# Kernel tuning notes

Measured on AMD Instinct MI355X. Metric: run time of the kernel, lower is better.

## Reference

```python
import jax, jax.numpy as jnp
import numpy as np

TEMP = 0.07
EPS = 1e-6

B = 8192
D1 = 129  # d+1 ambient Lorentz coords


def setup_inputs() -> dict:
    key = jax.random.key(0)
    k1, k2 = jax.random.split(key)
    z1 = jax.random.normal(k1, (B, D1), dtype=jnp.float32)
    z2 = jax.random.normal(k2, (B, D1), dtype=jnp.float32)
    return {"z1": z1, "z2": z2}


def _loss(z1, z2):
    # Minkowski (Lorentz) inner product via a single GEMM:
    # <x,y>_L = -x0*y0 + sum_i xi*yi  ->  x @ (metric * y)^T
    metric = jnp.concatenate([-jnp.ones((1,), z1.dtype), jnp.ones((D1 - 1,), z1.dtype)])
    inner = jnp.einsum('bd,kd->bk', z1, z2 * metric)  # (B, B)
    # Lorentz distance with curvature c=1: acosh(clamp(-<x,y>_L, 1+eps))
    dist = jnp.arccosh(jnp.clip(-inner, 1.0 + EPS, None))
    sims = -dist / TEMP
    # symmetric InfoNCE: labels are the diagonal
    logp_t2i = jax.nn.log_softmax(sims, axis=-1)      # text -> image
    logp_i2t = jax.nn.log_softmax(sims.T, axis=-1)    # image -> text
    diag = jnp.arange(sims.shape[0])
    loss_t2i = -jnp.mean(logp_t2i[diag, diag])
    loss_i2t = -jnp.mean(logp_i2t[diag, diag])
    return (loss_t2i + loss_i2t) / 2.0


def reference(z1, z2):
    return _loss(z1, z2)
```

## Files before the change

kernel.cpp:

```cpp
#include <hip/hip_runtime.h>
#include <math.h>


#define BDIM   8192
#define K_IN   129
#define K_PAD  160
#define BK     32
#define NKT    5
#define CTILES 8

typedef __bf16  bf16x8 __attribute__((ext_vector_type(8)));
typedef float   f32x4  __attribute__((ext_vector_type(4)));
typedef unsigned short u16x4 __attribute__((ext_vector_type(4)));

#define OFF_A    0u
#define OFF_B    (BDIM * K_PAD * 2u)
#define OFF_RS   (2u * BDIM * K_PAD * 2u)
#define OFF_CP   (OFF_RS + BDIM * 4u)
#define OFF_DG   (OFF_CP + 4u * BDIM * 4u)

__device__ __forceinline__ float fast_sqrt(float x) {
#if __has_builtin(__builtin_amdgcn_sqrtf)
    return __builtin_amdgcn_sqrtf(x);
#else
    return sqrtf(x);
#endif
}
__device__ __forceinline__ float fast_log2(float x) {
#if __has_builtin(__builtin_amdgcn_logf)
    return __builtin_amdgcn_logf(x);
#else
    return __log2f(x);
#endif
}
__device__ __forceinline__ float fast_exp2(float x) {
#if __has_builtin(__builtin_amdgcn_exp2f)
    return __builtin_amdgcn_exp2f(x);
#else
    extern "C" __device__ float __ocml_native_exp2_f32(float);
    return __ocml_native_exp2_f32(x);
#endif
}

__device__ __forceinline__ unsigned short f2bf_rne(float f) {
    unsigned int u = __float_as_uint(f);
    u += 0x7FFFu + ((u >> 16) & 1u);
    return (unsigned short)(u >> 16);
}

__global__ __launch_bounds__(256) void convert_kernel(
    const float* __restrict__ z1, const float* __restrict__ z2,
    unsigned short* __restrict__ A, unsigned short* __restrict__ B,
    float* __restrict__ rs_cp)
{
    int v = blockIdx.x * 256 + threadIdx.x;
    if (v < 5 * BDIM) rs_cp[v] = 0.f;
    if (v >= BDIM * (K_PAD / 4)) return;
    int r  = v / (K_PAD / 4);
    int c4 = (v - r * (K_PAD / 4)) * 4;
    u16x4 a, b;
    #pragma unroll
    for (int i = 0; i < 4; ++i) {
        int c = c4 + i;
        float va = 0.f, vb = 0.f;
        if (c < K_IN) {
            va = z1[r * K_IN + c];
            vb = z2[r * K_IN + c];
            if (c == 0) va = -va;
        }
        a[i] = f2bf_rne(va);
        b[i] = f2bf_rne(vb);
    }
    *(u16x4*)(A + r * K_PAD + c4) = a;
    *(u16x4*)(B + r * K_PAD + c4) = b;
}


#define STAGE(bufidx, cb)                                                     \
    {                                                                         \
        const char* _gp = (const char*)(B + (size_t)(cb) * K_PAD)             \
                          + lane * 16;                                        \
        char* _lp = (char*)&Bs[bufidx][0];                                    \
        __builtin_amdgcn_global_load_lds(                                     \
            (const __attribute__((address_space(1))) void*)                   \
                (_gp + wave * 1024),                                          \
            (__attribute__((address_space(3))) void*)(_lp + wave * 1024),     \
            16, 0, 0);                                                        \
        __builtin_amdgcn_global_load_lds(                                     \
            (const __attribute__((address_space(1))) void*)                   \
                (_gp + (wave + 8) * 1024),                                    \
            (__attribute__((address_space(3))) void*)(_lp + (wave + 8) * 1024),\
            16, 0, 0);                                                        \
        if (wave < 4)                                                         \
            __builtin_amdgcn_global_load_lds(                                 \
                (const __attribute__((address_space(1))) void*)               \
                    (_gp + (wave + 16) * 1024),                               \
                (__attribute__((address_space(3))) void*)(_lp + (wave + 16) * 1024),\
                16, 0, 0);                                                    \
    }

#define COMPUTE(bufidx, cb)                                                   \
    {                                                                         \
        const int colBase = (cb);                                             \
        const unsigned short* _Bt = &Bs[bufidx][0];                           \
        f32x4 acc[2][4] = {};                                                 \
        _Pragma("unroll")                                                     \
        for (int kt = 0; kt < NKT; ++kt) {                                    \
            bf16x8 bfr[4];                                                    \
            _Pragma("unroll")                                                 \
            for (int j = 0; j < 4; ++j)                                       \
                bfr[j] = *(const bf16x8*)                                     \
                    &_Bt[(l16 + j * 16) * K_PAD + quad * 8 + kt * BK];        \
            _Pragma("unroll")                                                 \
            for (int i = 0; i < 2; ++i)                                       \
                _Pragma("unroll")                                             \
                for (int j = 0; j < 4; ++j)                                   \
                    acc[i][j] = __builtin_amdgcn_mfma_f32_16x16x32_bf16(      \
                        Ah[i][kt], bfr[j], acc[i][j], 0, 0, 0);               \
        }                                                                     \
        const bool diagTile = (colBase == (rowBase & ~63));                   \
        const int  dj       = (rowBase >> 4) & 2;                             \
        float colp[4] = {0.f, 0.f, 0.f, 0.f};                                 \
        _Pragma("unroll")                                                     \
        for (int i = 0; i < 2; ++i) {                                         \
            _Pragma("unroll")                                                 \
            for (int j = 0; j < 4; ++j) {                                     \
                _Pragma("unroll")                                             \
                for (int reg = 0; reg < 4; ++reg) {                           \
                    float inner = acc[i][j][reg];                             \
                    float x = fmaxf(-inner, 1.000001f);                       \
                    float s = fast_sqrt(__builtin_fmaf(x, x, -1.0f));         \
                    float l2u = fast_log2(x + s);                             \
                    float e = fast_exp2(-14.285714285714286f * l2u);          \
                    rowp[i][reg] += e;                                        \
                    colp[j]      += e;                                        \
                    if (diagTile && (j - i) == dj && (quad * 4 + reg) == l16){\
                        int R = rowBase + i * 16 + quad * 4 + reg;            \
                        diag[R] = -9.902102579427789f * l2u;                  \
                    }                                                         \
                }                                                             \
            }                                                                 \
        }                                                                     \
        _Pragma("unroll")                                                     \
        for (int j = 0; j < 4; ++j) {                                         \
            float v = colp[j];                                                \
            v += __shfl_xor(v, 16);                                           \
            v += __shfl_xor(v, 32);                                           \
            if (quad == 0)                                                    \
                atomicAdd(&colRep[colBase + j * 16 + l16], v);                \
        }                                                                     \
    }

__global__ __launch_bounds__(512, 4) void gemm_epilogue_kernel(
    const unsigned short* __restrict__ A, const unsigned short* __restrict__ B,
    float* __restrict__ row_sum, float* __restrict__ col_part,
    float* __restrict__ diag)
{
    const int t    = threadIdx.x;
    const int lane = t & 63;
    const int wave = t >> 6;
    const int quad = lane >> 4;
    const int l16  = lane & 15;

    const int strip = blockIdx.x & 31;
    const int chunk = blockIdx.x >> 5;
    const int rowBase  = strip * 256 + wave * 32;
    const int colChunk = chunk * 512;

    const unsigned short* Abase = A + (rowBase + l16) * K_PAD + quad * 8;
    float* colRep = col_part + (strip & 3) * BDIM;

    __shared__ __align__(16) unsigned short Bs[2][64 * K_PAD];

    bf16x8 Ah[2][NKT];
    #pragma unroll
    for (int i = 0; i < 2; ++i)
        #pragma unroll
        for (int kt = 0; kt < NKT; ++kt)
            Ah[i][kt] = *(const bf16x8*)(Abase + i * 16 * K_PAD + kt * BK);

    float rowp[2][4] = {};

    STAGE(0, colChunk);
    __syncthreads();

    #pragma unroll 1
    for (int ct = 0; ct < CTILES; ++ct) {
        if (ct + 1 < CTILES)
            STAGE((ct + 1) & 1, colChunk + (ct + 1) * 64);
        COMPUTE(ct & 1, colChunk + ct * 64);
        __syncthreads();
    }

    #pragma unroll
    for (int i = 0; i < 2; ++i) {
        #pragma unroll
        for (int reg = 0; reg < 4; ++reg) {
            float v = rowp[i][reg];
            v += __shfl_xor(v, 1);
            v += __shfl_xor(v, 2);
            v += __shfl_xor(v, 4);
            v += __shfl_xor(v, 8);
            if (l16 == 0)
                atomicAdd(&row_sum[rowBase + i * 16 + quad * 4 + reg], v);
        }
    }
}

__global__ __launch_bounds__(1024) void finalize_kernel(
    const float* __restrict__ rs, const float* __restrict__ cp,
    const float* __restrict__ dg, float* __restrict__ out)
{
    __shared__ float part[16];
    int t = threadIdx.x;
    float a = 0.f;
    const float LN2_HALF = 0.34657359027997264f;
    for (int b = t; b < BDIM; b += 1024) {
        float cs = cp[b] + cp[b + BDIM] + cp[b + 2 * BDIM] + cp[b + 3 * BDIM];
        a += LN2_HALF * (fast_log2(rs[b]) + fast_log2(cs)) - dg[b];
    }
    #pragma unroll
    for (int m = 1; m < 64; m <<= 1) a += __shfl_xor(a, m);
    if ((t & 63) == 0) part[t >> 6] = a;
    __syncthreads();
    if (t < 16) {
        float v = part[t];
        #pragma unroll
        for (int m = 1; m < 16; m <<= 1) v += __shfl_xor(v, m);
        if (t == 0) out[0] = v * (1.0f / (float)BDIM);
    }
}

extern "C" void kernel_launch(void* const* d_in, const int* in_sizes, int n_in,
                              void* d_out, int out_size, void* d_ws, size_t ws_size,
                              hipStream_t stream)
{
    const float* z1 = (const float*)d_in[0];
    const float* z2 = (const float*)d_in[1];
    float* out = (float*)d_out;

    char* ws = (char*)d_ws;
    unsigned short* A  = (unsigned short*)(ws + OFF_A);
    unsigned short* B  = (unsigned short*)(ws + OFF_B);
    float* row_sum     = (float*)(ws + OFF_RS);
    float* col_part    = (float*)(ws + OFF_CP);
    float* diag        = (float*)(ws + OFF_DG);

    convert_kernel<<<(BDIM * (K_PAD / 4) + 255) / 256, 256, 0, stream>>>(
        z1, z2, A, B, row_sum );

    gemm_epilogue_kernel<<<512, 512, 0, stream>>>(
        A, B, row_sum, col_part, diag);

    finalize_kernel<<<1, 1024, 0, stream>>>(row_sum, col_part, diag, out);
}
```

Measured before the change: 108.7 us.

## Fuse convert, GEMM epilogue and finalize into one persistent kernel with grid barriers

Merges the three kernel launches into a single 512-block kernel. The kernel converts inputs to bf16 with a grid-stride loop, waits at a software grid barrier, runs the GEMM/epilogue, waits at a second barrier, and then computes a distributed final reduction with an atomicAdd into the output. The goal is to remove launch gaps and the single-block finalize tail. In exchange it adds a hipMemsetAsync for the barrier counters and relies on all 512 blocks being co-resident, otherwise the barrier spin deadlocks.

After: 199.5 us. 83.5% more time.

```diff
diff --git a/kernel.cpp b/kernel.cpp
--- a/kernel.cpp
+++ b/kernel.cpp
@@ -8,6 +8,8 @@
 #define BK     32
 #define NKT    5
 #define CTILES 8
+#define GRID   512
+#define NTHR   512
 
 typedef __bf16  bf16x8 __attribute__((ext_vector_type(8)));
 typedef float   f32x4  __attribute__((ext_vector_type(4)));
@@ -18,6 +20,7 @@
 #define OFF_RS   (2u * BDIM * K_PAD * 2u)
 #define OFF_CP   (OFF_RS + BDIM * 4u)
 #define OFF_DG   (OFF_CP + 4u * BDIM * 4u)
+#define OFF_SYNC (OFF_DG + BDIM * 4u)
 
 __device__ __forceinline__ float fast_sqrt(float x) {
 #if __has_builtin(__builtin_amdgcn_sqrtf)
@@ -48,37 +51,23 @@
     return (unsigned short)(u >> 16);
 }
 
-__global__ __launch_bounds__(256) void convert_kernel(
-    const float* __restrict__ z1, const float* __restrict__ z2,
-    unsigned short* __restrict__ A, unsigned short* __restrict__ B,
-    float* __restrict__ rs_cp)
-{
-    int v = blockIdx.x * 256 + threadIdx.x;
-    if (v < 5 * BDIM) rs_cp[v] = 0.f;
-    if (v >= BDIM * (K_PAD / 4)) return;
-    int r  = v / (K_PAD / 4);
-    int c4 = (v - r * (K_PAD / 4)) * 4;
-    u16x4 a, b;
-    #pragma unroll
-    for (int i = 0; i < 4; ++i) {
-        int c = c4 + i;
-        float va = 0.f, vb = 0.f;
-        if (c < K_IN) {
-            va = z1[r * K_IN + c];
-            vb = z2[r * K_IN + c];
-            if (c == 0) va = -va;
-        }
-        a[i] = f2bf_rne(va);
-        b[i] = f2bf_rne(vb);
-    }
-    *(u16x4*)(A + r * K_PAD + c4) = a;
-    *(u16x4*)(B + r * K_PAD + c4) = b;
+__device__ __forceinline__ void grid_barrier(unsigned int* cnt) {
+    __syncthreads();
+    if (threadIdx.x == 0) {
+        __threadfence();
+        atomicAdd(cnt, 1u);
+        while (__hip_atomic_load(cnt, __ATOMIC_RELAXED,
+                                 __HIP_MEMORY_SCOPE_AGENT) < GRID)
+            __builtin_amdgcn_s_sleep(2);
+        __threadfence();
+    }
+    __syncthreads();
 }
 
 
 #define STAGE(bufidx, cb)                                                     \
     {                                                                         \
-        const char* _gp = (const char*)(B + (size_t)(cb) * K_PAD)             \
+        const char* _gp = (const char*)(Bp + (size_t)(cb) * K_PAD)            \
                           + lane * 16;                                        \
         char* _lp = (char*)&Bs[bufidx][0];                                    \
         __builtin_amdgcn_global_load_lds(                                     \
@@ -151,83 +140,108 @@
         }                                                                     \
     }
 
-__global__ __launch_bounds__(512, 4) void gemm_epilogue_kernel(
-    const unsigned short* __restrict__ A, const unsigned short* __restrict__ B,
+__global__ __launch_bounds__(NTHR, 4) void fused_kernel(
+    const float* __restrict__ z1, const float* __restrict__ z2,
+    unsigned short* __restrict__ A, unsigned short* __restrict__ Bp,
     float* __restrict__ row_sum, float* __restrict__ col_part,
-    float* __restrict__ diag)
+    float* __restrict__ diag, unsigned int* __restrict__ sync0,
+    unsigned int* __restrict__ sync1, float* __restrict__ out)
 {
-    const int t    = threadIdx.x;
-    const int lane = t & 63;
-    const int wave = t >> 6;
-    const int quad = lane >> 4;
-    const int l16  = lane & 15;
-
-    const int strip = blockIdx.x & 31;
-    const int chunk = blockIdx.x >> 5;
-    const int rowBase  = strip * 256 + wave * 32;
-    const int colChunk = chunk * 512;
-
-    const unsigned short* Abase = A + (rowBase + l16) * K_PAD + quad * 8;
-    float* colRep = col_part + (strip & 3) * BDIM;
-
-    __shared__ __align__(16) unsigned short Bs[2][64 * K_PAD];
-
-    bf16x8 Ah[2][NKT];
-    #pragma unroll
-    for (int i = 0; i < 2; ++i)
+    const int t   = threadIdx.x;
+    const int bid = blockIdx.x;
+
+    {
+        int tidg = bid * NTHR + t;
+        if (tidg < 5 * BDIM) row_sum[tidg] = 0.f;
+        if (tidg == 0) out[0] = 0.f;
+        for (int v = tidg; v < BDIM * (K_PAD / 4); v += GRID * NTHR) {
+            int r  = v / (K_PAD / 4);
+            int c4 = (v - r * (K_PAD / 4)) * 4;
+            u16x4 a, b;
+            #pragma unroll
+            for (int i = 0; i < 4; ++i) {
+                int c = c4 + i;
+                float va = 0.f, vb = 0.f;
+                if (c < K_IN) {
+                    va = z1[r * K_IN + c];
+                    vb = z2[r * K_IN + c];
+                    if (c == 0) va = -va;
+                }
+                a[i] = f2bf_rne(va);
+                b[i] = f2bf_rne(vb);
+            }
+            *(u16x4*)(A + r * K_PAD + c4)  = a;
+            *(u16x4*)(Bp + r * K_PAD + c4) = b;
+        }
+    }
+
+    grid_barrier(sync0);
+
+    {
+        const int lane = t & 63;
+        const int wave = t >> 6;
+        const int quad = lane >> 4;
+        const int l16  = lane & 15;
+
+        const int strip = bid & 31;
+        const int chunk = bid >> 5;
+        const int rowBase  = strip * 256 + wave * 32;
+        const int colChunk = chunk * 512;
+
+        const unsigned short* Abase = A + (rowBase + l16) * K_PAD + quad * 8;
+        float* colRep = col_part + (strip & 3) * BDIM;
+
+        __shared__ __align__(16) unsigned short Bs[2][64 * K_PAD];
+
+        bf16x8 Ah[2][NKT];
         #pragma unroll
-        for (int kt = 0; kt < NKT; ++kt)
-            Ah[i][kt] = *(const bf16x8*)(Abase + i * 16 * K_PAD + kt * BK);
-
-    float rowp[2][4] = {};
-
-    STAGE(0, colChunk);
-    __syncthreads();
-
-    #pragma unroll 1
-    for (int ct = 0; ct < CTILES; ++ct) {
-        if (ct + 1 < CTILES)
-            STAGE((ct + 1) & 1, colChunk + (ct + 1) * 64);
-        COMPUTE(ct & 1, colChunk + ct * 64);
+        for (int i = 0; i < 2; ++i)
+            #pragma unroll
+            for (int kt = 0; kt < NKT; ++kt)
+                Ah[i][kt] = *(const bf16x8*)(Abase + i * 16 * K_PAD + kt * BK);
+
+        float rowp[2][4] = {};
+
+        STAGE(0, colChunk);
         __syncthreads();
-    }
-
-    #pragma unroll
-    for (int i = 0; i < 2; ++i) {
+
+        #pragma unroll 1
+        for (int ct = 0; ct < CTILES; ++ct) {
+            if (ct + 1 < CTILES)
+                STAGE((ct + 1) & 1, colChunk + (ct + 1) * 64);
+            COMPUTE(ct & 1, colChunk + ct * 64);
+            __syncthreads();
+        }
+
         #pragma unroll
-        for (int reg = 0; reg < 4; ++reg) {
-            float v = rowp[i][reg];
-            v += __shfl_xor(v, 1);
-            v += __shfl_xor(v, 2);
-            v += __shfl_xor(v, 4);
-            v += __shfl_xor(v, 8);
-            if (l16 == 0)
-                atomicAdd(&row_sum[rowBase + i * 16 + quad * 4 + reg], v);
+        for (int i = 0; i < 2; ++i) {
+            #pragma unroll
+            for (int reg = 0; reg < 4; ++reg) {
+                float v = rowp[i][reg];
+                v += __shfl_xor(v, 1);
+                v += __shfl_xor(v, 2);
+                v += __shfl_xor(v, 4);
+                v += __shfl_xor(v, 8);
+                if (l16 == 0)
+                    atomicAdd(&row_sum[rowBase + i * 16 + quad * 4 + reg], v);
+            }
         }
     }
-}
-
-__global__ __launch_bounds__(1024) void finalize_kernel(
-    const float* __restrict__ rs, const float* __restrict__ cp,
-    const float* __restrict__ dg, float* __restrict__ out)
-{
-    __shared__ float part[16];
-    int t = threadIdx.x;
-    float a = 0.f;
-    const float LN2_HALF = 0.34657359027997264f;
-    for (int b = t; b < BDIM; b += 1024) {
-        float cs = cp[b] + cp[b + BDIM] + cp[b + 2 * BDIM] + cp[b + 3 * BDIM];
-        a += LN2_HALF * (fast_log2(rs[b]) + fast_log2(cs)) - dg[b];
-    }
-    #pragma unroll
-    for (int m = 1; m < 64; m <<= 1) a += __shfl_xor(a, m);
-    if ((t & 63) == 0) part[t >> 6] = a;
-    __syncthreads();
+
+    grid_barrier(sync1);
+
     if (t < 16) {
-        float v = part[t];
-        #pragma unroll
-        for (int m = 1; m < 16; m <<= 1) v += __shfl_xor(v, m);
-        if (t == 0) out[0] = v * (1.0f / (float)BDIM);
+        const float LN2_HALF = 0.34657359027997264f;
+        int b = bid * 16 + t;
+        float cs = col_part[b] + col_part[b + BDIM] +
+                   col_part[b + 2 * BDIM] + col_part[b + 3 * BDIM];
+        float a = LN2_HALF * (fast_log2(row_sum[b]) + fast_log2(cs)) - diag[b];
+        a += __shfl_xor(a, 1);
+        a += __shfl_xor(a, 2);
+        a += __shfl_xor(a, 4);
+        a += __shfl_xor(a, 8);
+        if (t == 0)
+            atomicAdd(out, a * (1.0f / (float)BDIM));
     }
 }
 
@@ -245,12 +259,10 @@
     float* row_sum     = (float*)(ws + OFF_RS);
     float* col_part    = (float*)(ws + OFF_CP);
     float* diag        = (float*)(ws + OFF_DG);
-
-    convert_kernel<<<(BDIM * (K_PAD / 4) + 255) / 256, 256, 0, stream>>>(
-        z1, z2, A, B, row_sum );
-
-    gemm_epilogue_kernel<<<512, 512, 0, stream>>>(
-        A, B, row_sum, col_part, diag);
-
-    finalize_kernel<<<1, 1024, 0, stream>>>(row_sum, col_part, diag, out);
-}
+    unsigned int* sync = (unsigned int*)(ws + OFF_SYNC);
+
+    hipMemsetAsync(sync, 0, 2 * sizeof(unsigned int), stream);
+
+    fused_kernel<<<GRID, NTHR, 0, stream>>>(
+        z1, z2, A, B, row_sum, col_part, diag, sync, sync + 1, out);
+}
```
